# Kernel tuning notes

Measured on AMD Instinct MI355X. Metric: run time of the kernel, lower is better.

## Reference

```python
import jax, jax.numpy as jnp
import numpy as np


def setup_inputs() -> dict:
    key = jax.random.key(0)
    k_x, k_c = jax.random.split(key)
    ROWS, COLS = 4, 4
    B, N = 1024, 224
    x = jax.random.normal(k_x, (B, N, N), dtype=jnp.float32)
    # kaiming_normal_ on [rows, cols]: std = sqrt(2 / fan_in) with fan_in = cols
    coef = jax.random.normal(k_c, (ROWS, COLS), dtype=jnp.float32) * np.sqrt(2.0 / COLS)
    return {"x": x, "coef": coef}


def reference(x, coef):
    # x: [B, N, N]; coef: [rows, cols]
    rows, cols = coef.shape
    B, N, _ = x.shape

    # a_series[i] = matrix_power(x, i+2) for i in 0..rows-1 (the original also
    # computes power rows+2 but never uses it). Only the diagonals are needed:
    # diag(A ** p) == diag(A) ** p for elementwise power p.
    def step(P, _):
        Pn = jnp.matmul(P, x)                      # next matrix power, [B, N, N]
        return Pn, jnp.diagonal(Pn, axis1=-2, axis2=-1)  # [B, N]

    _, diags = jax.lax.scan(step, x, None, length=rows)  # [rows, B, N]
    d = jnp.transpose(diags, (1, 0, 2))                  # [B, rows, N]

    # traces[b, i, j] = sum_n diag(x^{i+2})[b, n] ** (j+1)
    exps = jnp.arange(1, cols + 1)                       # [cols]
    traces = jnp.sum(d[..., None] ** exps, axis=2)       # [B, rows, cols]

    # norm[i, j] = (N*N) ** (i + j + 2), computed in float (the original's int64
    # pow overflows for any realistic N; float is the intended math)
    i = jnp.arange(rows, dtype=x.dtype)[:, None]
    j = jnp.arange(cols, dtype=x.dtype)[None, :]
    norm = jnp.asarray(float(N * N), x.dtype) ** (i + j + 2.0)  # [rows, cols]

    return jnp.sum(coef * traces / norm, axis=(-1, -2))  # [B]
```

## Files before the change

### kernel.cpp

```cpp
#include <hip/hip_runtime.h>
#include <stdint.h>

#define B_ 1024
#define N_ 224
#define TS 112
#define KB 16

__device__ __forceinline__ void gload16(const void* g, void* l) {
  __builtin_amdgcn_global_load_lds(
      (const __attribute__((address_space(1))) uint32_t*)g,
      (__attribute__((address_space(3))) uint32_t*)l,
      16, 0, 0);
}

__global__ __launch_bounds__(256) void gemm224(const float* __restrict__ Ag,
                                               const float* __restrict__ Bg,
                                               float* __restrict__ Cg) {
  __shared__ __align__(16) float As[2][TS * KB];
  __shared__ __align__(16) float Bs[2][KB * TS];

  const size_t mo = (size_t)blockIdx.z * (N_ * N_);
  const float* A = Ag + mo;
  const float* Bm = Bg + mo;
  float* C = Cg + mo;
  const int m0 = blockIdx.x * TS;
  const int n0 = blockIdx.y * TS;
  const int t = threadIdx.x;
  const int tx = t & 15, ty = t >> 4;

  const int f1 = t + 256;
  const size_t aOff0 = (size_t)(m0 + (t >> 2)) * N_ + ((t & 3) << 2);
  const size_t bOff0 = (size_t)(t / 28) * N_ + n0 + (t % 28) * 4;
  const size_t aOff1 = (size_t)(m0 + (f1 >> 2)) * N_ + ((f1 & 3) << 2);
  const size_t bOff1 = (size_t)(f1 / 28) * N_ + n0 + (f1 % 28) * 4;
  const int l0 = t << 2;
  const int l1 = f1 << 2;

  float acc[7][7] = {};

  auto stage = [&](int buf, int k0) {
    gload16(A + aOff0 + k0, &As[buf][l0]);
    gload16(Bm + bOff0 + (size_t)k0 * N_, &Bs[buf][l0]);
    if (f1 < 448) {
      gload16(A + aOff1 + k0, &As[buf][l1]);
      gload16(Bm + bOff1 + (size_t)k0 * N_, &Bs[buf][l1]);
    }
  };

  stage(0, 0);
  int cur = 0;
  for (int kt = 0; kt < N_ / KB; ++kt) {
    __syncthreads();
    if (kt + 1 < N_ / KB) stage(cur ^ 1, (kt + 1) * KB);
    const float* Asb = As[cur];
    const float* Bsb = Bs[cur];
#pragma unroll
    for (int k = 0; k < KB; ++k) {
      float a[7], bv[7];
#pragma unroll
      for (int i = 0; i < 7; ++i) a[i] = Asb[(ty + (i << 4)) * KB + k];
#pragma unroll
      for (int j = 0; j < 7; ++j) bv[j] = Bsb[k * TS + tx + (j << 4)];
#pragma unroll
      for (int i = 0; i < 7; ++i)
#pragma unroll
        for (int j = 0; j < 7; ++j) acc[i][j] = fmaf(a[i], bv[j], acc[i][j]);
    }
    cur ^= 1;
  }

#pragma unroll
  for (int i = 0; i < 7; ++i) {
    float* crow = C + (size_t)(m0 + ty + (i << 4)) * N_ + n0 + tx;
#pragma unroll
    for (int j = 0; j < 7; ++j) crow[j << 4] = acc[i][j];
  }
}

__global__ __launch_bounds__(256) void diagk(const float* __restrict__ P2g,
                                             const float* __restrict__ P3g,
                                             float* __restrict__ dg, int bBase) {
  __shared__ float s2[N_][KB + 1];
  __shared__ float s3[N_][KB + 1];
  const int b = blockIdx.x;
  const float* p2 = P2g + (size_t)b * N_ * N_;
  const float* p3 = P3g + (size_t)b * N_ * N_;
  const int gb = bBase + b;
  const int t = threadIdx.x;
  float d4 = 0.f, d5 = 0.f;
  for (int kb = 0; kb < N_; kb += KB) {
    __syncthreads();
#pragma unroll
    for (int base = 0; base < N_ * KB; base += 256) {
      int f = base + t;
      int n = f >> 4, j = f & 15;
      s2[n][j] = p2[(size_t)n * N_ + kb + j];
      s3[n][j] = p3[(size_t)n * N_ + kb + j];
    }
    __syncthreads();
    if (t < N_) {
#pragma unroll
      for (int j = 0; j < KB; ++j) {
        float c2 = p2[(size_t)(kb + j) * N_ + t];
        d4 = fmaf(s2[t][j], c2, d4);
        d5 = fmaf(s3[t][j], c2, d5);
      }
    }
  }
  if (t < N_) {
    dg[((size_t)0 * B_ + gb) * N_ + t] = p2[(size_t)t * N_ + t];
    dg[((size_t)1 * B_ + gb) * N_ + t] = p3[(size_t)t * N_ + t];
    dg[((size_t)2 * B_ + gb) * N_ + t] = d4;
    dg[((size_t)3 * B_ + gb) * N_ + t] = d5;
  }
}

__global__ __launch_bounds__(256) void combine(const float* __restrict__ dg,
                                               const float* __restrict__ coef,
                                               float* __restrict__ out) {
  const int lane = threadIdx.x & 63;
  const int b = blockIdx.x * 4 + (threadIdx.x >> 6);
  float T[4][4] = {};
  for (int n = lane; n < N_; n += 64) {
#pragma unroll
    for (int i = 0; i < 4; ++i) {
      float d = dg[((size_t)i * B_ + b) * N_ + n];
      float p = d;
#pragma unroll
      for (int j = 0; j < 4; ++j) {
        T[i][j] += p;
        p *= d;
      }
    }
  }
#pragma unroll
  for (int i = 0; i < 4; ++i)
#pragma unroll
    for (int j = 0; j < 4; ++j)
#pragma unroll
      for (int s = 32; s > 0; s >>= 1) T[i][j] += __shfl_xor(T[i][j], s, 64);
  if (lane == 0) {
    double acc = 0.0;
#pragma unroll
    for (int i = 0; i < 4; ++i)
#pragma unroll
      for (int j = 0; j < 4; ++j) {
        double norm = 1.0;
        for (int e = 0; e < i + j + 2; ++e) norm *= (double)(N_ * N_);
        acc += (double)coef[i * 4 + j] * ((double)T[i][j] / norm);
      }
    out[b] = (float)acc;
  }
}

extern "C" void kernel_launch(void* const* d_in, const int* in_sizes, int n_in,
                              void* d_out, int out_size, void* d_ws, size_t ws_size,
                              hipStream_t stream) {
  (void)in_sizes; (void)n_in; (void)out_size;
  const float* x = (const float*)d_in[0];
  const float* coef = (const float*)d_in[1];
  float* out = (float*)d_out;
  char* ws = (char*)d_ws;

  const size_t diagBytes = (size_t)4 * B_ * N_ * sizeof(float);
  float* dg = (float*)ws;
  const size_t perMat = (size_t)N_ * N_ * sizeof(float);
  size_t rem = (ws_size > diagBytes + 256) ? (ws_size - diagBytes - 256) : 0;
  long long Cc = (long long)(rem / (2 * perMat));
  if (Cc < 1) Cc = 1;
  if (Cc > B_) Cc = B_;
  const int C = (int)Cc;
  float* P2 = (float*)(ws + ((diagBytes + 255) & ~(size_t)255));
  float* P3 = P2 + (size_t)C * N_ * N_;

  for (int b0 = 0; b0 < B_; b0 += C) {
    const int cb = (B_ - b0 < C) ? (B_ - b0) : C;
    const float* xc = x + (size_t)b0 * N_ * N_;
    dim3 g(2, 2, cb);
    gemm224<<<g, 256, 0, stream>>>(xc, xc, P2);
    gemm224<<<g, 256, 0, stream>>>(P2, xc, P3);
    diagk<<<cb, 256, 0, stream>>>(P2, P3, dg, b0);
  }
  combine<<<256, 256, 0, stream>>>(dg, coef, out);
}
```

Before: 1.110 ms.

## Use split-bf16 MFMA GEMMs with pre-transposed hi/lo operands for matrix powers

Replaces the scalar fp32 FMA GEMM with an MFMA 16x16x32 bf16 kernel. It keeps fp32-like accuracy by splitting each operand into high and low bf16 parts and summing three cross products. A new splitT kernel produces hi/lo copies of x plus transposed copies, so both GEMM operands load row-contiguous into XOR-swizzled LDS. Blocks are remapped for XCD locality, and the 224-wide output is covered by overlapping 128-row tiles. The extra split pass, the hi/lo intermediate storage and reduced precision in the diagonal reconstruction are the trade-offs.

```diff
diff --git a/kernel.cpp b/kernel.cpp
--- a/kernel.cpp
+++ b/kernel.cpp
@@ -3,113 +3,179 @@
 
 #define B_ 1024
 #define N_ 224
-#define TS 112
-#define KB 16
+#define NN_ (N_ * N_)
+
+typedef unsigned short u16;
+typedef unsigned int u32;
+typedef __attribute__((ext_vector_type(8))) short s8v;
+typedef __attribute__((ext_vector_type(4))) float f4v;
+
+__device__ __forceinline__ u16 f2bf(float f) {
+  u32 u = __float_as_uint(f);
+  u = (u + 0x7FFFu + ((u >> 16) & 1u)) >> 16;
+  return (u16)u;
+}
+__device__ __forceinline__ float bf2f(u16 h) { return __uint_as_float((u32)h << 16); }
+__device__ __forceinline__ float rec(u16 h, u16 l) { return bf2f(h) + bf2f(l); }
 
 __device__ __forceinline__ void gload16(const void* g, void* l) {
   __builtin_amdgcn_global_load_lds(
       (const __attribute__((address_space(1))) uint32_t*)g,
-      (__attribute__((address_space(3))) uint32_t*)l,
-      16, 0, 0);
-}
-
-__global__ __launch_bounds__(256) void gemm224(const float* __restrict__ Ag,
-                                               const float* __restrict__ Bg,
-                                               float* __restrict__ Cg) {
-  __shared__ __align__(16) float As[2][TS * KB];
-  __shared__ __align__(16) float Bs[2][KB * TS];
-
-  const size_t mo = (size_t)blockIdx.z * (N_ * N_);
-  const float* A = Ag + mo;
-  const float* Bm = Bg + mo;
-  float* C = Cg + mo;
-  const int m0 = blockIdx.x * TS;
-  const int n0 = blockIdx.y * TS;
+      (__attribute__((address_space(3))) uint32_t*)l, 16, 0, 0);
+}
+
+__global__ __launch_bounds__(256) void splitT(const float* __restrict__ x,
+                                              u16* __restrict__ xh, u16* __restrict__ xl,
+                                              u16* __restrict__ xhT, u16* __restrict__ xlT) {
+  __shared__ u16 th[32][34];
+  __shared__ u16 tl[32][34];
+  const int bid = blockIdx.x;
+  const int mat = bid / 49, t2 = bid % 49;
+  const int tm = (t2 / 7) * 32, tn = (t2 % 7) * 32;
   const int t = threadIdx.x;
-  const int tx = t & 15, ty = t >> 4;
-
-  const int f1 = t + 256;
-  const size_t aOff0 = (size_t)(m0 + (t >> 2)) * N_ + ((t & 3) << 2);
-  const size_t bOff0 = (size_t)(t / 28) * N_ + n0 + (t % 28) * 4;
-  const size_t aOff1 = (size_t)(m0 + (f1 >> 2)) * N_ + ((f1 & 3) << 2);
-  const size_t bOff1 = (size_t)(f1 / 28) * N_ + n0 + (f1 % 28) * 4;
-  const int l0 = t << 2;
-  const int l1 = f1 << 2;
-
-  float acc[7][7] = {};
+  const int r = t >> 3, c4 = (t & 7) << 2;
+  const size_t o = (size_t)mat * NN_ + (size_t)(tm + r) * N_ + tn + c4;
+  const float4 v = *(const float4*)(x + o);
+  u16 h0 = f2bf(v.x), h1 = f2bf(v.y), h2 = f2bf(v.z), h3 = f2bf(v.w);
+  u16 l0 = f2bf(v.x - bf2f(h0)), l1 = f2bf(v.y - bf2f(h1));
+  u16 l2 = f2bf(v.z - bf2f(h2)), l3 = f2bf(v.w - bf2f(h3));
+  ushort4 hv = {h0, h1, h2, h3}, lv = {l0, l1, l2, l3};
+  *(ushort4*)(xh + o) = hv;
+  *(ushort4*)(xl + o) = lv;
+  th[r][c4] = h0; th[r][c4 + 1] = h1; th[r][c4 + 2] = h2; th[r][c4 + 3] = h3;
+  tl[r][c4] = l0; tl[r][c4 + 1] = l1; tl[r][c4 + 2] = l2; tl[r][c4 + 3] = l3;
+  __syncthreads();
+  ushort4 thv = {th[c4][r], th[c4 + 1][r], th[c4 + 2][r], th[c4 + 3][r]};
+  ushort4 tlv = {tl[c4][r], tl[c4 + 1][r], tl[c4 + 2][r], tl[c4 + 3][r]};
+  const size_t oT = (size_t)mat * NN_ + (size_t)(tn + r) * N_ + tm + c4;
+  *(ushort4*)(xhT + oT) = thv;
+  *(ushort4*)(xlT + oT) = tlv;
+}
+
+__global__ __launch_bounds__(256, 2) void gemmNT(const u16* __restrict__ Ah, const u16* __restrict__ Al,
+                                                 const u16* __restrict__ BTh, const u16* __restrict__ BTl,
+                                                 u16* __restrict__ Ch, u16* __restrict__ Cl) {
+  __shared__ __align__(16) u16 As[2][128][64];
+  __shared__ __align__(16) u16 Bs[2][128][64];
+
+  const int nwg = gridDim.x, bid = blockIdx.x;
+  const int q = nwg >> 3, rr = nwg & 7, xcd = bid & 7, pos = bid >> 3;
+  const int wg = (xcd < rr) ? (xcd * (q + 1) + pos) : (rr * (q + 1) + (xcd - rr) * q + pos);
+  const int mat = wg >> 2, t2 = wg & 3;
+  const int m0 = (t2 & 1) * 96, n0 = (t2 >> 1) * 96;
+  const size_t mo = (size_t)mat * NN_;
+  const u16* A0 = Ah + mo;
+  const u16* A1 = Al + mo;
+  const u16* B0 = BTh + mo;
+  const u16* B1 = BTl + mo;
+
+  const int t = threadIdx.x;
+  const int l = t & 63, w = t >> 6;
+  const int wm = w & 1, wn = w >> 1;
+  const int lg = l >> 4, l15 = l & 15;
+
+  f4v acc[4][4];
+#pragma unroll
+  for (int i = 0; i < 4; ++i)
+#pragma unroll
+    for (int j = 0; j < 4; ++j) acc[i][j] = (f4v){0.f, 0.f, 0.f, 0.f};
 
   auto stage = [&](int buf, int k0) {
-    gload16(A + aOff0 + k0, &As[buf][l0]);
-    gload16(Bm + bOff0 + (size_t)k0 * N_, &Bs[buf][l0]);
-    if (f1 < 448) {
-      gload16(A + aOff1 + k0, &As[buf][l1]);
-      gload16(Bm + bOff1 + (size_t)k0 * N_, &Bs[buf][l1]);
+#pragma unroll
+    for (int i = 0; i < 4; ++i) {
+      const int s = i * 256 + t;
+      const int row = s >> 3, p = s & 7;
+      const int c = p ^ (row & 7);
+      const int g = c & 3;
+      const u16* ga = (c < 4) ? A0 : A1;
+      const u16* gb = (c < 4) ? B0 : B1;
+      gload16(ga + (size_t)(m0 + row) * N_ + k0 + g * 8, &As[buf][row][p * 8]);
+      gload16(gb + (size_t)(n0 + row) * N_ + k0 + g * 8, &Bs[buf][row][p * 8]);
     }
   };
 
   stage(0, 0);
   int cur = 0;
-  for (int kt = 0; kt < N_ / KB; ++kt) {
+  for (int kt = 0; kt < 7; ++kt) {
     __syncthreads();
-    if (kt + 1 < N_ / KB) stage(cur ^ 1, (kt + 1) * KB);
-    const float* Asb = As[cur];
-    const float* Bsb = Bs[cur];
-#pragma unroll
-    for (int k = 0; k < KB; ++k) {
-      float a[7], bv[7];
-#pragma unroll
-      for (int i = 0; i < 7; ++i) a[i] = Asb[(ty + (i << 4)) * KB + k];
-#pragma unroll
-      for (int j = 0; j < 7; ++j) bv[j] = Bsb[k * TS + tx + (j << 4)];
-#pragma unroll
-      for (int i = 0; i < 7; ++i)
-#pragma unroll
-        for (int j = 0; j < 7; ++j) acc[i][j] = fmaf(a[i], bv[j], acc[i][j]);
-    }
+    if (kt < 6) stage(cur ^ 1, (kt + 1) * 32);
+    const u16(*Ab)[64] = As[cur];
+    const u16(*Bb)[64] = Bs[cur];
+    s8v ah[4], al[4], bh[4], bl[4];
+#pragma unroll
+    for (int i = 0; i < 4; ++i) {
+      const int ra = wm * 64 + i * 16 + l15;
+      const int rb = wn * 64 + i * 16 + l15;
+      ah[i] = *(const s8v*)&Ab[ra][(lg ^ (ra & 7)) * 8];
+      al[i] = *(const s8v*)&Ab[ra][((4 + lg) ^ (ra & 7)) * 8];
+      bh[i] = *(const s8v*)&Bb[rb][(lg ^ (rb & 7)) * 8];
+      bl[i] = *(const s8v*)&Bb[rb][((4 + lg) ^ (rb & 7)) * 8];
+    }
+#pragma unroll
+    for (int i = 0; i < 4; ++i)
+#pragma unroll
+      for (int j = 0; j < 4; ++j) {
+        acc[i][j] = __builtin_amdgcn_mfma_f32_16x16x32_bf16(ah[i], bh[j], acc[i][j], 0, 0, 0);
+        acc[i][j] = __builtin_amdgcn_mfma_f32_16x16x32_bf16(ah[i], bl[j], acc[i][j], 0, 0, 0);
+        acc[i][j] = __builtin_amdgcn_mfma_f32_16x16x32_bf16(al[i], bh[j], acc[i][j], 0, 0, 0);
+      }
     cur ^= 1;
   }
 
-#pragma unroll
-  for (int i = 0; i < 7; ++i) {
-    float* crow = C + (size_t)(m0 + ty + (i << 4)) * N_ + n0 + tx;
-#pragma unroll
-    for (int j = 0; j < 7; ++j) crow[j << 4] = acc[i][j];
-  }
-}
-
-__global__ __launch_bounds__(256) void diagk(const float* __restrict__ P2g,
-                                             const float* __restrict__ P3g,
+  u16* cph = Ch + mo;
+  u16* cpl = Cl + mo;
+#pragma unroll
+  for (int i = 0; i < 4; ++i)
+#pragma unroll
+    for (int j = 0; j < 4; ++j)
+#pragma unroll
+      for (int qd = 0; qd < 4; ++qd) {
+        const float v = acc[i][j][qd];
+        const int row = m0 + wm * 64 + i * 16 + lg * 4 + qd;
+        const int col = n0 + wn * 64 + j * 16 + l15;
+        const u16 hh = f2bf(v);
+        const u16 ll = f2bf(v - bf2f(hh));
+        cph[(size_t)row * N_ + col] = hh;
+        cpl[(size_t)row * N_ + col] = ll;
+      }
+}
+
+__global__ __launch_bounds__(256) void diagk(const u16* __restrict__ P2h, const u16* __restrict__ P2l,
+                                             const u16* __restrict__ P3h, const u16* __restrict__ P3l,
                                              float* __restrict__ dg, int bBase) {
-  __shared__ float s2[N_][KB + 1];
-  __shared__ float s3[N_][KB + 1];
+  __shared__ float s2[N_][17];
+  __shared__ float s3[N_][17];
   const int b = blockIdx.x;
-  const float* p2 = P2g + (size_t)b * N_ * N_;
-  const float* p3 = P3g + (size_t)b * N_ * N_;
+  const size_t mo = (size_t)b * NN_;
+  const u16 *p2h = P2h + mo, *p2l = P2l + mo, *p3h = P3h + mo, *p3l = P3l + mo;
   const int gb = bBase + b;
   const int t = threadIdx.x;
   float d4 = 0.f, d5 = 0.f;
-  for (int kb = 0; kb < N_; kb += KB) {
+  for (int kb = 0; kb < N_; kb += 16) {
     __syncthreads();
 #pragma unroll
-    for (int base = 0; base < N_ * KB; base += 256) {
-      int f = base + t;
-      int n = f >> 4, j = f & 15;
-      s2[n][j] = p2[(size_t)n * N_ + kb + j];
-      s3[n][j] = p3[(size_t)n * N_ + kb + j];
+    for (int base = 0; base < N_ * 16; base += 256) {
+      const int f = base + t;
+      const int n = f >> 4, j = f & 15;
+      const size_t idx = (size_t)n * N_ + kb + j;
+      s2[n][j] = rec(p2h[idx], p2l[idx]);
+      s3[n][j] = rec(p3h[idx], p3l[idx]);
     }
     __syncthreads();
     if (t < N_) {
 #pragma unroll
-      for (int j = 0; j < KB; ++j) {
-        float c2 = p2[(size_t)(kb + j) * N_ + t];
+      for (int j = 0; j < 16; ++j) {
+        const size_t ci = (size_t)(kb + j) * N_ + t;
+        const float c2 = rec(p2h[ci], p2l[ci]);
         d4 = fmaf(s2[t][j], c2, d4);
         d5 = fmaf(s3[t][j], c2, d5);
       }
     }
   }
   if (t < N_) {
-    dg[((size_t)0 * B_ + gb) * N_ + t] = p2[(size_t)t * N_ + t];
-    dg[((size_t)1 * B_ + gb) * N_ + t] = p3[(size_t)t * N_ + t];
+    const size_t di = (size_t)t * N_ + t;
+    dg[((size_t)0 * B_ + gb) * N_ + t] = rec(p2h[di], p2l[di]);
+    dg[((size_t)1 * B_ + gb) * N_ + t] = rec(p3h[di], p3l[di]);
     dg[((size_t)2 * B_ + gb) * N_ + t] = d4;
     dg[((size_t)3 * B_ + gb) * N_ + t] = d5;
   }
@@ -124,7 +190,7 @@
   for (int n = lane; n < N_; n += 64) {
 #pragma unroll
     for (int i = 0; i < 4; ++i) {
-      float d = dg[((size_t)i * B_ + b) * N_ + n];
+      const float d = dg[((size_t)i * B_ + b) * N_ + n];
       float p = d;
 #pragma unroll
       for (int j = 0; j < 4; ++j) {
@@ -162,24 +228,38 @@
   float* out = (float*)d_out;
   char* ws = (char*)d_ws;
 
-  const size_t diagBytes = (size_t)4 * B_ * N_ * sizeof(float);
-  float* dg = (float*)ws;
-  const size_t perMat = (size_t)N_ * N_ * sizeof(float);
-  size_t rem = (ws_size > diagBytes + 256) ? (ws_size - diagBytes - 256) : 0;
-  long long Cc = (long long)(rem / (2 * perMat));
+  size_t off = 0;
+  auto alloc = [&](size_t bytes) -> void* {
+    off = (off + 255) & ~(size_t)255;
+    void* p = ws + off;
+    off += bytes;
+    return p;
+  };
+
+  float* dg = (float*)alloc((size_t)4 * B_ * N_ * sizeof(float));
+
+  const size_t perMat = (size_t)8 * NN_ * sizeof(u16);
+  size_t avail = (ws_size > off + 256) ? (ws_size - off - 256) : 0;
+  long long Cc = (long long)(avail / perMat);
   if (Cc < 1) Cc = 1;
   if (Cc > B_) Cc = B_;
   const int C = (int)Cc;
-  float* P2 = (float*)(ws + ((diagBytes + 255) & ~(size_t)255));
-  float* P3 = P2 + (size_t)C * N_ * N_;
+  const size_t matEls = (size_t)C * NN_;
+  u16* xh = (u16*)alloc(matEls * 2);
+  u16* xl = (u16*)alloc(matEls * 2);
+  u16* xhT = (u16*)alloc(matEls * 2);
+  u16* xlT = (u16*)alloc(matEls * 2);
+  u16* P2h = (u16*)alloc(matEls * 2);
+  u16* P2l = (u16*)alloc(matEls * 2);
+  u16* P3h = (u16*)alloc(matEls * 2);
+  u16* P3l = (u16*)alloc(matEls * 2);
 
   for (int b0 = 0; b0 < B_; b0 += C) {
     const int cb = (B_ - b0 < C) ? (B_ - b0) : C;
-    const float* xc = x + (size_t)b0 * N_ * N_;
-    dim3 g(2, 2, cb);
-    gemm224<<<g, 256, 0, stream>>>(xc, xc, P2);
-    gemm224<<<g, 256, 0, stream>>>(P2, xc, P3);
-    diagk<<<cb, 256, 0, stream>>>(P2, P3, dg, b0);
+    splitT<<<49 * cb, 256, 0, stream>>>(x + (size_t)b0 * NN_, xh, xl, xhT, xlT);
+    gemmNT<<<4 * cb, 256, 0, stream>>>(xh, xl, xhT, xlT, P2h, P2l);
+    gemmNT<<<4 * cb, 256, 0, stream>>>(P2h, P2l, xhT, xlT, P3h, P3l);
+    diagk<<<cb, 256, 0, stream>>>(P2h, P2l, P3h, P3l, dg, b0);
   }
   combine<<<256, 256, 0, stream>>>(dg, coef, out);
 }
```

Result: no change. 1.117 ms (+0.6%).
